# Performance work log

Measured on AMD Instinct MI355X. Metric: run time of the kernel, lower is better.

The kernel has to match this reference:

```python
import jax, jax.numpy as jnp
import numpy as np
import math

B, Q_LEN, PAST, HID = 1, 1024, 3072, 4096
NH, NKV, HD = 32, 8, 128
KV_LEN = PAST + Q_LEN
ROPE_THETA = 10000.0


def setup_inputs() -> dict:
    key = jax.random.key(0)
    ks = jax.random.split(key, 8)
    s = 0.02
    hidden_states = jax.random.normal(ks[0], (B, Q_LEN, HID), jnp.float32)
    # additive causal mask with KV cache offset: query i attends keys j <= PAST + i
    i = jnp.arange(Q_LEN)[:, None]
    j = jnp.arange(KV_LEN)[None, :]
    attention_mask = jnp.where(j <= PAST + i, 0.0, -1e9).astype(jnp.float32)[None, None]
    position_ids = (jnp.arange(Q_LEN, dtype=jnp.int64) + PAST)[None, :]
    past_k = jax.random.normal(ks[1], (B, NKV, PAST, HD), jnp.float32)
    past_v = jax.random.normal(ks[2], (B, NKV, PAST, HD), jnp.float32)
    Wq = jax.random.normal(ks[3], (NH * HD, HID), jnp.float32) * s
    Wk = jax.random.normal(ks[4], (NKV * HD, HID), jnp.float32) * s
    Wv = jax.random.normal(ks[5], (NKV * HD, HID), jnp.float32) * s
    Wo = jax.random.normal(ks[6], (HID, NH * HD), jnp.float32) * s
    return {"hidden_states": hidden_states, "attention_mask": attention_mask,
            "position_ids": position_ids, "past_k": past_k, "past_v": past_v,
            "Wq": Wq, "Wk": Wk, "Wv": Wv, "Wo": Wo}


def _rope_tables(seq_len, head_dim, dtype):
    inv_freq = 1.0 / (ROPE_THETA ** (jnp.arange(0, head_dim, 2, dtype=jnp.float32) / head_dim))
    t = jnp.arange(seq_len, dtype=jnp.float32)
    freqs = jnp.outer(t, inv_freq)            # [seq, hd/2]
    emb = jnp.concatenate([freqs, freqs], -1)  # [seq, hd]
    return jnp.cos(emb).astype(dtype), jnp.sin(emb).astype(dtype)


def _rotate_half(x):
    x1, x2 = jnp.split(x, 2, axis=-1)
    return jnp.concatenate([-x2, x1], axis=-1)


def reference(hidden_states, attention_mask, position_ids, past_k, past_v, Wq, Wk, Wv, Wo):
    bsz, q_len, _ = hidden_states.shape
    q = (hidden_states @ Wq.T).reshape(bsz, q_len, NH, HD).transpose(0, 2, 1, 3)
    k = (hidden_states @ Wk.T).reshape(bsz, q_len, NKV, HD).transpose(0, 2, 1, 3)
    v = (hidden_states @ Wv.T).reshape(bsz, q_len, NKV, HD).transpose(0, 2, 1, 3)

    kv_seq_len = q_len + past_k.shape[2]
    cos_t, sin_t = _rope_tables(kv_seq_len, HD, q.dtype)
    cos = cos_t[position_ids][:, None]  # [b,1,q,hd]
    sin = sin_t[position_ids][:, None]
    q = q * cos + _rotate_half(q) * sin
    k = k * cos + _rotate_half(k) * sin

    k = jnp.concatenate([past_k, k], axis=2)  # [b,nkv,kv,hd]
    v = jnp.concatenate([past_v, v], axis=2)
    n_rep = NH // NKV
    k = jnp.repeat(k, n_rep, axis=1)  # GQA repeat_kv -> [b,nh,kv,hd]
    v = jnp.repeat(v, n_rep, axis=1)

    scores = jnp.einsum('bhqd,bhkd->bhqk', q, k) / math.sqrt(HD)
    scores = scores + attention_mask
    weights = jax.nn.softmax(scores.astype(jnp.float32), axis=-1).astype(q.dtype)
    attn = jnp.einsum('bhqk,bhkd->bhqd', weights, v)
    attn = attn.transpose(0, 2, 1, 3).reshape(bsz, q_len, NH * HD)
    return attn @ Wo.T
```

## Files before the change

### kernel.cpp

```cpp
#include <hip/hip_runtime.h>

#define QLEN 1024
#define PASTN 3072
#define KVLEN 4096
#define HIDN 4096
#define NHEAD 32
#define NKVH 8
#define HDIM 128
#define NQKVC 6144

typedef unsigned short u16;
typedef __bf16 bf16x8 __attribute__((ext_vector_type(8)));
typedef float f32x4 __attribute__((ext_vector_type(4)));
typedef float f32x16 __attribute__((ext_vector_type(16)));
typedef u16 us8 __attribute__((ext_vector_type(8)));
typedef u16 us4 __attribute__((ext_vector_type(4)));

__device__ __forceinline__ u16 f2bf(float x) {
  unsigned u = __builtin_bit_cast(unsigned, x);
  u += 0x7fffu + ((u >> 16) & 1u);
  return (u16)(u >> 16);
}
__device__ __forceinline__ float bf2f(u16 b) {
  return __builtin_bit_cast(float, (unsigned)b << 16);
}

#define GLL16(gp, lp) __builtin_amdgcn_global_load_lds( \
    (const __attribute__((address_space(1))) void*)(gp), \
    (__attribute__((address_space(3))) void*)(lp), 16, 0, 0)

__global__ __launch_bounds__(256) void cvt_kernel(const float* __restrict__ src,
                                                  u16* __restrict__ dst, int n) {
  int i = (blockIdx.x * 256 + threadIdx.x) * 4;
  if (i >= n) return;
  float4 f = *(const float4*)(src + i);
  ushort4 o = make_ushort4(f2bf(f.x), f2bf(f.y), f2bf(f.z), f2bf(f.w));
  *(ushort4*)(dst + i) = o;
}

__device__ __forceinline__ void storeC(float* p, float v) { *p = v; }
__device__ __forceinline__ void storeC(u16* p, float v) { *p = f2bf(v); }

template <typename CT>
__global__ __launch_bounds__(256) void gemm_bt(const u16* __restrict__ A,
                                               const u16* __restrict__ B,
                                               CT* __restrict__ C, int M, int N, int K) {
  __shared__ u16 Alds[2][64 * 32];
  __shared__ u16 Blds[2][128 * 32];
  const int tid = threadIdx.x, wid = tid >> 6, lane = tid & 63;
  const int m0 = blockIdx.y * 64, n0 = blockIdx.x * 128;
  const int wm = (wid >> 1) * 32, wn = (wid & 1) * 64;
  const int l15 = lane & 15, l4 = lane >> 4;
  const int srow = lane >> 2, sp = lane & 3;
  f32x4 acc[2][4] = {};
  auto stage = [&](int buf, int kt) {
    {
      const int r = wid * 16 + srow;
      GLL16(A + (size_t)(m0 + r) * K + kt + (sp ^ ((r >> 1) & 3)) * 8,
            &Alds[buf][wid * 512]);
    }
#pragma unroll
    for (int i = 0; i < 2; ++i) {
      const int c = wid * 2 + i;
      const int r = c * 16 + srow;
      GLL16(B + (size_t)(n0 + r) * K + kt + (sp ^ ((r >> 1) & 3)) * 8,
            &Blds[buf][c * 512]);
    }
  };
  stage(0, 0);
  __syncthreads();
  int cur = 0;
  for (int kt = 0; kt < K; kt += 32) {
    if (kt + 32 < K) stage(cur ^ 1, kt + 32);
    bf16x8 a[2], b[4];
#pragma unroll
    for (int i = 0; i < 2; ++i) {
      const int R = wm + i * 16 + l15;
      a[i] = *(const bf16x8*)&Alds[cur][R * 32 + (l4 ^ ((R >> 1) & 3)) * 8];
    }
#pragma unroll
    for (int j = 0; j < 4; ++j) {
      const int R = wn + j * 16 + l15;
      b[j] = *(const bf16x8*)&Blds[cur][R * 32 + (l4 ^ ((R >> 1) & 3)) * 8];
    }
#pragma unroll
    for (int i = 0; i < 2; ++i)
#pragma unroll
      for (int j = 0; j < 4; ++j)
        acc[i][j] = __builtin_amdgcn_mfma_f32_16x16x32_bf16(a[i], b[j], acc[i][j], 0, 0, 0);
    __syncthreads();
    cur ^= 1;
  }
#pragma unroll
  for (int i = 0; i < 2; ++i)
#pragma unroll
    for (int j = 0; j < 4; ++j) {
      int row = m0 + wm + i * 16 + l4 * 4;
      int col = n0 + wn + j * 16 + l15;
#pragma unroll
      for (int r = 0; r < 4; ++r) storeC(&C[(size_t)(row + r) * N + col], acc[i][j][r]);
    }
}

__global__ __launch_bounds__(256) void rope_q_kernel(const u16* __restrict__ qkv,
                                                     u16* __restrict__ qr) {
  int idx = blockIdx.x * 256 + threadIdx.x;
  int i = idx & 63, h = (idx >> 6) & 31, r = idx >> 11;
  float freq = __expf(-(float)i * (9.210340371976184f / 64.f));
  float angle = (float)(PASTN + r) * freq;
  float sn, cs;
  sincosf(angle, &sn, &cs);
  int base = r * NQKVC + h * HDIM + i;
  float x1 = bf2f(qkv[base]);
  float x2 = bf2f(qkv[base + 64]);
  int ob = r * HIDN + h * HDIM + i;
  qr[ob] = f2bf(x1 * cs - x2 * sn);
  qr[ob + 64] = f2bf(x2 * cs + x1 * sn);
}

__global__ __launch_bounds__(256) void repack_k_kernel(const float* __restrict__ past_k,
                                                       const u16* __restrict__ qkv,
                                                       u16* __restrict__ kb) {
  int idx = blockIdx.x * 256 + threadIdx.x;
  int d = idx & 127, kv = (idx >> 7) & 4095, hk = idx >> 19;
  float val;
  if (kv < PASTN) {
    val = past_k[((size_t)hk * PASTN + kv) * HDIM + d];
  } else {
    int r = kv - PASTN;
    float x = bf2f(qkv[(size_t)r * NQKVC + 4096 + hk * HDIM + d]);
    float xp = bf2f(qkv[(size_t)r * NQKVC + 4096 + hk * HDIM + (d ^ 64)]);
    int i = d & 63;
    float freq = __expf(-(float)i * (9.210340371976184f / 64.f));
    float angle = (float)(PASTN + r) * freq;
    float sn, cs;
    sincosf(angle, &sn, &cs);
    val = (d < 64) ? (x * cs - xp * sn) : (x * cs + xp * sn);
  }
  kb[idx] = f2bf(val);
}

__global__ __launch_bounds__(256) void repack_vt_kernel(const float* __restrict__ past_v,
                                                        const u16* __restrict__ qkv,
                                                        u16* __restrict__ vtb) {
  __shared__ u16 tile[32][136];
  int hk = blockIdx.y, kv0 = blockIdx.x * 32, tid = threadIdx.x;
  int j = tid >> 3, d0 = (tid & 7) * 16;
  if (kv0 < PASTN) {
    const float* src = past_v + ((size_t)hk * PASTN + kv0 + j) * HDIM + d0;
#pragma unroll
    for (int x = 0; x < 16; x += 4) {
      float4 f = *(const float4*)(src + x);
      tile[j][d0 + x] = f2bf(f.x);
      tile[j][d0 + x + 1] = f2bf(f.y);
      tile[j][d0 + x + 2] = f2bf(f.z);
      tile[j][d0 + x + 3] = f2bf(f.w);
    }
  } else {
    int r = kv0 - PASTN + j;
    const u16* src = qkv + (size_t)r * NQKVC + 5120 + hk * HDIM + d0;
    *(us8*)&tile[j][d0] = *(const us8*)src;
    *(us8*)&tile[j][d0 + 8] = *(const us8*)(src + 8);
  }
  __syncthreads();
  int d = tid >> 1, jb = (tid & 1) * 16;
  us8 o0, o1;
#pragma unroll
  for (int x = 0; x < 8; ++x) {
    o0[x] = tile[jb + x][d];
    o1[x] = tile[jb + 8 + x][d];
  }
  u16* dst = vtb + ((size_t)hk * HDIM + d) * KVLEN + kv0 + jb;
  *(us8*)dst = o0;
  *(us8*)(dst + 8) = o1;
}

__global__ __launch_bounds__(128) void attn_kernel(const u16* __restrict__ q,
                                                   const u16* __restrict__ kc,
                                                   const u16* __restrict__ vt,
                                                   float* __restrict__ opart,
                                                   float* __restrict__ mlbuf) {
  __shared__ u16 Klds[64 * 128];
  __shared__ u16 Vlds[128 * 64];
  const int tid = threadIdx.x, wid = tid >> 6, lane = tid & 63;
  const int l31 = lane & 31, hi = lane >> 5, l15 = lane & 15;
  const int h = blockIdx.y, hk = h >> 2;
  const int q0 = blockIdx.x * 64;
  const int z = blockIdx.z;
  const int pid = h * 16 + blockIdx.x;
  const int qrow = q0 + wid * 32 + l31;
  bf16x8 qf[8];
  {
    const u16* qp = q + (size_t)qrow * HIDN + h * HDIM + hi * 8;
#pragma unroll
    for (int dk = 0; dk < 8; ++dk) qf[dk] = *(const bf16x8*)(qp + dk * 16);
  }
  float m_run = -1e30f, l_run = 0.f;
  f32x16 oacc[4] = {};
  const u16* kbase = kc + (size_t)hk * KVLEN * HDIM;
  const u16* vbase = vt + (size_t)hk * HDIM * KVLEN;
  const int ntiles = (PASTN + q0 + 64) >> 6;
  const int half = ntiles >> 1;
  const int t0 = z ? half : 0, t1 = z ? ntiles : half;
  const float C = 0.12753102f;
  const int qpos = PASTN + qrow;
  for (int t = t0; t < t1; ++t) {
    const int kv0 = t << 6;
    {
#pragma unroll
      for (int i = 0; i < 8; ++i) {
        const int w = wid * 8 + i;
        const int p = w * 4 + (lane >> 4);
        const int key = (p & 0x33) | ((p & 4) << 1) | ((p & 8) >> 1);
        const int sl = (lane & 15) ^ (p & 15);
        GLL16(kbase + (size_t)(kv0 + key) * HDIM + sl * 8, &Klds[w * 512]);
      }
#pragma unroll
      for (int i = 0; i < 8; ++i) {
        const int w = wid * 8 + i;
        const int d = w * 8 + (lane >> 3);
        const int sl = (lane & 7) ^ ((lane >> 3) & 7);
        GLL16(vbase + (size_t)d * KVLEN + kv0 + sl * 8, &Vlds[w * 512]);
      }
    }
    __syncthreads();
    f32x16 s[2] = {};
    __builtin_amdgcn_s_setprio(1);
#pragma unroll
    for (int tt = 0; tt < 2; ++tt)
#pragma unroll
      for (int dk = 0; dk < 8; ++dk) {
        const int idx = (tt * 32 + l31) * 128 + (((dk * 2 + hi) ^ l15) * 8);
        bf16x8 kf = *(const bf16x8*)&Klds[idx];
        s[tt] = __builtin_amdgcn_mfma_f32_32x32x16_bf16(kf, qf[dk], s[tt], 0, 0, 0);
      }
    __builtin_amdgcn_s_setprio(0);
    float pm = -1e30f;
    if (t == ntiles - 1) {
#pragma unroll
      for (int tt = 0; tt < 2; ++tt)
#pragma unroll
        for (int reg = 0; reg < 16; ++reg) {
          const int key = kv0 + tt * 32 + (reg & 7) + 8 * hi + ((reg & 8) << 1);
          float v = s[tt][reg] * C;
          if (key > qpos) v = -1e30f;
          s[tt][reg] = v;
          pm = fmaxf(pm, v);
        }
    } else {
#pragma unroll
      for (int tt = 0; tt < 2; ++tt)
#pragma unroll
        for (int reg = 0; reg < 16; ++reg) {
          float v = s[tt][reg] * C;
          s[tt][reg] = v;
          pm = fmaxf(pm, v);
        }
    }
    pm = fmaxf(pm, __shfl_xor(pm, 32));
    if (!__all(pm <= m_run)) {
      const float mn = fmaxf(m_run, pm);
      const float corr = exp2f(m_run - mn);
      m_run = mn;
      l_run *= corr;
#pragma unroll
      for (int db = 0; db < 4; ++db)
#pragma unroll
        for (int r = 0; r < 16; ++r) oacc[db][r] *= corr;
    }
    float rs = 0.f;
#pragma unroll
    for (int tt = 0; tt < 2; ++tt)
#pragma unroll
      for (int reg = 0; reg < 16; ++reg) {
        const float p = exp2f(s[tt][reg] - m_run);
        s[tt][reg] = p;
        rs += p;
      }
    rs += __shfl_xor(rs, 32);
    l_run += rs;
    __builtin_amdgcn_s_setprio(1);
#pragma unroll
    for (int kc2 = 0; kc2 < 4; ++kc2) {
      bf16x8 pa;
#pragma unroll
      for (int j = 0; j < 8; ++j) pa[j] = (__bf16)s[kc2 >> 1][(kc2 & 1) * 8 + j];
#pragma unroll
      for (int db = 0; db < 4; ++db) {
        const int idx = (db * 32 + l31) * 64 + (((kc2 * 2 + hi) ^ (l31 & 7)) * 8);
        bf16x8 vf = *(const bf16x8*)&Vlds[idx];
        oacc[db] = __builtin_amdgcn_mfma_f32_32x32x16_bf16(vf, pa, oacc[db], 0, 0, 0);
      }
    }
    __builtin_amdgcn_s_setprio(0);
    __syncthreads();
  }
  const int orow = wid * 32 + l31;
  float* op = opart + (size_t)(z * 512 + pid) * (64 * 128) + orow * 128;
#pragma unroll
  for (int db = 0; db < 4; ++db)
#pragma unroll
    for (int g = 0; g < 4; ++g) {
      f32x4 w4;
#pragma unroll
      for (int j = 0; j < 4; ++j) w4[j] = oacc[db][g * 4 + j];
      *(f32x4*)&op[db * 32 + g * 8 + hi * 4] = w4;
    }
  if (hi == 0) {
    float* mlp = mlbuf + (size_t)((z * 512 + pid) * 64 + orow) * 2;
    mlp[0] = m_run;
    mlp[1] = l_run;
  }
}

__global__ __launch_bounds__(256) void attn_combine(const float* __restrict__ opart,
                                                    const float* __restrict__ mlbuf,
                                                    u16* __restrict__ o) {
  const int pid = blockIdx.x;
  const int h = pid >> 4, qt = pid & 15;
  const int q = threadIdx.x >> 2, dc = (threadIdx.x & 3) * 32;
  const float* ml0 = mlbuf + (size_t)(pid * 64 + q) * 2;
  const float* ml1 = mlbuf + (size_t)((512 + pid) * 64 + q) * 2;
  const float m0 = ml0[0], l0 = ml0[1], m1 = ml1[0], l1 = ml1[1];
  const float m = fmaxf(m0, m1);
  const float w0 = exp2f(m0 - m), w1 = exp2f(m1 - m);
  const float inv = 1.f / (w0 * l0 + w1 * l1);
  const float* O0 = opart + (size_t)pid * (64 * 128) + q * 128 + dc;
  const float* O1 = opart + (size_t)(512 + pid) * (64 * 128) + q * 128 + dc;
  u16* dst = o + (size_t)(qt * 64 + q) * HIDN + h * HDIM + dc;
#pragma unroll
  for (int x = 0; x < 8; ++x) {
    f32x4 a = *(const f32x4*)(O0 + x * 4);
    f32x4 b = *(const f32x4*)(O1 + x * 4);
    us4 w4;
#pragma unroll
    for (int j = 0; j < 4; ++j) w4[j] = f2bf((a[j] * w0 + b[j] * w1) * inv);
    *(us4*)(dst + x * 4) = w4;
  }
}

extern "C" void kernel_launch(void* const* d_in, const int* in_sizes, int n_in,
                              void* d_out, int out_size, void* d_ws, size_t ws_size,
                              hipStream_t stream) {
  (void)in_sizes; (void)n_in; (void)out_size; (void)ws_size;
  const float* hidden = (const float*)d_in[0];
  const float* past_k = (const float*)d_in[3];
  const float* past_v = (const float*)d_in[4];
  const float* Wq = (const float*)d_in[5];
  const float* Wk = (const float*)d_in[6];
  const float* Wv = (const float*)d_in[7];
  const float* Wo = (const float*)d_in[8];
  float* out = (float*)d_out;

  char* w = (char*)d_ws;
  u16* hiddenb = (u16*)w; w += (size_t)QLEN * HIDN * 2;
  u16* wqkv    = (u16*)w; w += (size_t)NQKVC * HIDN * 2;
  u16* wo      = (u16*)w; w += (size_t)HIDN * HIDN * 2;
  u16* qkvraw  = (u16*)w; w += (size_t)QLEN * NQKVC * 2;
  u16* qrope   = (u16*)w; w += (size_t)QLEN * HIDN * 2;
  u16* kbuf    = (u16*)w; w += (size_t)NKVH * KVLEN * HDIM * 2;
  u16* vtbuf   = (u16*)w; w += (size_t)NKVH * HDIM * KVLEN * 2;
  u16* attnb   = (u16*)w; w += (size_t)QLEN * HIDN * 2;
  float* opart = (float*)wqkv;
  float* mlbuf = opart + (size_t)2 * 512 * 64 * 128;

  cvt_kernel<<<(QLEN * HIDN) / 1024, 256, 0, stream>>>(hidden, hiddenb, QLEN * HIDN);
  cvt_kernel<<<(NHEAD * HDIM * HIDN) / 1024, 256, 0, stream>>>(Wq, wqkv, NHEAD * HDIM * HIDN);
  cvt_kernel<<<(NKVH * HDIM * HIDN) / 1024, 256, 0, stream>>>(Wk, wqkv + (size_t)4096 * HIDN,
                                                              NKVH * HDIM * HIDN);
  cvt_kernel<<<(NKVH * HDIM * HIDN) / 1024, 256, 0, stream>>>(Wv, wqkv + (size_t)5120 * HIDN,
                                                              NKVH * HDIM * HIDN);
  cvt_kernel<<<(HIDN * HIDN) / 1024, 256, 0, stream>>>(Wo, wo, HIDN * HIDN);

  gemm_bt<u16><<<dim3(NQKVC / 128, QLEN / 64), 256, 0, stream>>>(hiddenb, wqkv, qkvraw,
                                                                 QLEN, NQKVC, HIDN);

  rope_q_kernel<<<(QLEN * NHEAD * 64) / 256, 256, 0, stream>>>(qkvraw, qrope);
  repack_k_kernel<<<(NKVH * KVLEN * HDIM) / 256, 256, 0, stream>>>(past_k, qkvraw, kbuf);
  repack_vt_kernel<<<dim3(KVLEN / 32, NKVH), 256, 0, stream>>>(past_v, qkvraw, vtbuf);

  attn_kernel<<<dim3(QLEN / 64, NHEAD, 2), 128, 0, stream>>>(qrope, kbuf, vtbuf,
                                                             opart, mlbuf);
  attn_combine<<<512, 256, 0, stream>>>(opart, mlbuf, attnb);

  gemm_bt<float><<<dim3(HIDN / 128, QLEN / 64), 256, 0, stream>>>(attnb, wo, out,
                                                                  QLEN, HIDN, HIDN);
}
```

Measured before the change: 381.9 us.

## Enlarge attention query tile to 256 rows and double-buffer K/V staging

Each attention block now handles 256 query rows with 8 waves instead of 64 rows with 2 waves, so every K/V tile staged in LDS is reused by four times as many queries. Global-to-LDS loads for the next tile are prefetched into a second LDS buffer while the current one is computed, overlapping load latency with MFMA work. The causal mask test now covers the last several tiles, because rows earlier in a larger block reach the diagonal sooner, and the combine kernel and partial-buffer layout are reshaped to match. In exchange, the grid shrinks to 256 blocks, roughly one per CU, which lowers latency hiding across blocks, and LDS use per block doubles.

```diff
diff --git a/kernel.cpp b/kernel.cpp
--- a/kernel.cpp
+++ b/kernel.cpp
@@ -175,19 +175,19 @@
   *(us8*)(dst + 8) = o1;
 }
 
-__global__ __launch_bounds__(128) void attn_kernel(const u16* __restrict__ q,
+__global__ __launch_bounds__(512) void attn_kernel(const u16* __restrict__ q,
                                                    const u16* __restrict__ kc,
                                                    const u16* __restrict__ vt,
                                                    float* __restrict__ opart,
                                                    float* __restrict__ mlbuf) {
-  __shared__ u16 Klds[64 * 128];
-  __shared__ u16 Vlds[128 * 64];
+  __shared__ u16 Klds[2][64 * 128];
+  __shared__ u16 Vlds[2][128 * 64];
   const int tid = threadIdx.x, wid = tid >> 6, lane = tid & 63;
   const int l31 = lane & 31, hi = lane >> 5, l15 = lane & 15;
   const int h = blockIdx.y, hk = h >> 2;
-  const int q0 = blockIdx.x * 64;
+  const int q0 = blockIdx.x * 256;
   const int z = blockIdx.z;
-  const int pid = h * 16 + blockIdx.x;
+  const int pid = h * 4 + blockIdx.x;
   const int qrow = q0 + wid * 32 + l31;
   bf16x8 qf[8];
   {
@@ -199,31 +199,36 @@
   f32x16 oacc[4] = {};
   const u16* kbase = kc + (size_t)hk * KVLEN * HDIM;
   const u16* vbase = vt + (size_t)hk * HDIM * KVLEN;
-  const int ntiles = (PASTN + q0 + 64) >> 6;
+  const int ntiles = (PASTN + q0 + 256) >> 6;
   const int half = ntiles >> 1;
   const int t0 = z ? half : 0, t1 = z ? ntiles : half;
   const float C = 0.12753102f;
   const int qpos = PASTN + qrow;
+  auto stage = [&](int buf, int kv0) {
+#pragma unroll
+    for (int i = 0; i < 2; ++i) {
+      const int w = wid * 2 + i;
+      const int p = w * 4 + (lane >> 4);
+      const int key = (p & 0x33) | ((p & 4) << 1) | ((p & 8) >> 1);
+      const int sl = (lane & 15) ^ (p & 15);
+      GLL16(kbase + (size_t)(kv0 + key) * HDIM + sl * 8, &Klds[buf][w * 512]);
+    }
+#pragma unroll
+    for (int i = 0; i < 2; ++i) {
+      const int w = wid * 2 + i;
+      const int d = w * 8 + (lane >> 3);
+      const int sl = (lane & 7) ^ ((lane >> 3) & 7);
+      GLL16(vbase + (size_t)d * KVLEN + kv0 + sl * 8, &Vlds[buf][w * 512]);
+    }
+  };
+  stage(0, t0 << 6);
+  __syncthreads();
+  int cur = 0;
   for (int t = t0; t < t1; ++t) {
+    if (t + 1 < t1) stage(cur ^ 1, (t + 1) << 6);
     const int kv0 = t << 6;
-    {
-#pragma unroll
-      for (int i = 0; i < 8; ++i) {
-        const int w = wid * 8 + i;
-        const int p = w * 4 + (lane >> 4);
-        const int key = (p & 0x33) | ((p & 4) << 1) | ((p & 8) >> 1);
-        const int sl = (lane & 15) ^ (p & 15);
-        GLL16(kbase + (size_t)(kv0 + key) * HDIM + sl * 8, &Klds[w * 512]);
-      }
-#pragma unroll
-      for (int i = 0; i < 8; ++i) {
-        const int w = wid * 8 + i;
-        const int d = w * 8 + (lane >> 3);
-        const int sl = (lane & 7) ^ ((lane >> 3) & 7);
-        GLL16(vbase + (size_t)d * KVLEN + kv0 + sl * 8, &Vlds[w * 512]);
-      }
-    }
-    __syncthreads();
+    const u16* Kb = Klds[cur];
+    const u16* Vb = Vlds[cur];
     f32x16 s[2] = {};
     __builtin_amdgcn_s_setprio(1);
 #pragma unroll
@@ -231,12 +236,12 @@
 #pragma unroll
       for (int dk = 0; dk < 8; ++dk) {
         const int idx = (tt * 32 + l31) * 128 + (((dk * 2 + hi) ^ l15) * 8);
-        bf16x8 kf = *(const bf16x8*)&Klds[idx];
+        bf16x8 kf = *(const bf16x8*)&Kb[idx];
         s[tt] = __builtin_amdgcn_mfma_f32_32x32x16_bf16(kf, qf[dk], s[tt], 0, 0, 0);
       }
     __builtin_amdgcn_s_setprio(0);
     float pm = -1e30f;
-    if (t == ntiles - 1) {
+    if (kv0 + 63 > PASTN + q0) {
 #pragma unroll
       for (int tt = 0; tt < 2; ++tt)
 #pragma unroll
@@ -288,15 +293,16 @@
 #pragma unroll
       for (int db = 0; db < 4; ++db) {
         const int idx = (db * 32 + l31) * 64 + (((kc2 * 2 + hi) ^ (l31 & 7)) * 8);
-        bf16x8 vf = *(const bf16x8*)&Vlds[idx];
+        bf16x8 vf = *(const bf16x8*)&Vb[idx];
         oacc[db] = __builtin_amdgcn_mfma_f32_32x32x16_bf16(vf, pa, oacc[db], 0, 0, 0);
       }
     }
     __builtin_amdgcn_s_setprio(0);
     __syncthreads();
+    cur ^= 1;
   }
   const int orow = wid * 32 + l31;
-  float* op = opart + (size_t)(z * 512 + pid) * (64 * 128) + orow * 128;
+  float* op = opart + ((size_t)(z * 128 + pid) * 256 + orow) * 128;
 #pragma unroll
   for (int db = 0; db < 4; ++db)
 #pragma unroll
@@ -307,7 +313,7 @@
       *(f32x4*)&op[db * 32 + g * 8 + hi * 4] = w4;
     }
   if (hi == 0) {
-    float* mlp = mlbuf + (size_t)((z * 512 + pid) * 64 + orow) * 2;
+    float* mlp = mlbuf + ((size_t)(z * 128 + pid) * 256 + orow) * 2;
     mlp[0] = m_run;
     mlp[1] = l_run;
   }
@@ -317,25 +323,29 @@
                                                     const float* __restrict__ mlbuf,
                                                     u16* __restrict__ o) {
   const int pid = blockIdx.x;
-  const int h = pid >> 4, qt = pid & 15;
-  const int q = threadIdx.x >> 2, dc = (threadIdx.x & 3) * 32;
-  const float* ml0 = mlbuf + (size_t)(pid * 64 + q) * 2;
-  const float* ml1 = mlbuf + (size_t)((512 + pid) * 64 + q) * 2;
-  const float m0 = ml0[0], l0 = ml0[1], m1 = ml1[0], l1 = ml1[1];
-  const float m = fmaxf(m0, m1);
-  const float w0 = exp2f(m0 - m), w1 = exp2f(m1 - m);
-  const float inv = 1.f / (w0 * l0 + w1 * l1);
-  const float* O0 = opart + (size_t)pid * (64 * 128) + q * 128 + dc;
-  const float* O1 = opart + (size_t)(512 + pid) * (64 * 128) + q * 128 + dc;
-  u16* dst = o + (size_t)(qt * 64 + q) * HIDN + h * HDIM + dc;
-#pragma unroll
-  for (int x = 0; x < 8; ++x) {
-    f32x4 a = *(const f32x4*)(O0 + x * 4);
-    f32x4 b = *(const f32x4*)(O1 + x * 4);
-    us4 w4;
-#pragma unroll
-    for (int j = 0; j < 4; ++j) w4[j] = f2bf((a[j] * w0 + b[j] * w1) * inv);
-    *(us4*)(dst + x * 4) = w4;
+  const int h = pid >> 2, qt = pid & 3;
+  const int q2 = threadIdx.x >> 2, dc = (threadIdx.x & 3) * 32;
+#pragma unroll
+  for (int b = 0; b < 4; ++b) {
+    const int q = b * 64 + q2;
+    const float* ml0 = mlbuf + ((size_t)pid * 256 + q) * 2;
+    const float* ml1 = mlbuf + ((size_t)(128 + pid) * 256 + q) * 2;
+    const float m0 = ml0[0], l0 = ml0[1], m1 = ml1[0], l1 = ml1[1];
+    const float m = fmaxf(m0, m1);
+    const float w0 = exp2f(m0 - m), w1 = exp2f(m1 - m);
+    const float inv = 1.f / (w0 * l0 + w1 * l1);
+    const float* O0 = opart + ((size_t)pid * 256 + q) * 128 + dc;
+    const float* O1 = opart + ((size_t)(128 + pid) * 256 + q) * 128 + dc;
+    u16* dst = o + (size_t)(qt * 256 + q) * HIDN + h * HDIM + dc;
+#pragma unroll
+    for (int x = 0; x < 8; ++x) {
+      f32x4 a = *(const f32x4*)(O0 + x * 4);
+      f32x4 bb = *(const f32x4*)(O1 + x * 4);
+      us4 w4;
+#pragma unroll
+      for (int j = 0; j < 4; ++j) w4[j] = f2bf((a[j] * w0 + bb[j] * w1) * inv);
+      *(us4*)(dst + x * 4) = w4;
+    }
   }
 }
 
@@ -362,7 +372,7 @@
   u16* vtbuf   = (u16*)w; w += (size_t)NKVH * HDIM * KVLEN * 2;
   u16* attnb   = (u16*)w; w += (size_t)QLEN * HIDN * 2;
   float* opart = (float*)wqkv;
-  float* mlbuf = opart + (size_t)2 * 512 * 64 * 128;
+  float* mlbuf = opart + (size_t)2 * 128 * 256 * 128;
 
   cvt_kernel<<<(QLEN * HIDN) / 1024, 256, 0, stream>>>(hidden, hiddenb, QLEN * HIDN);
   cvt_kernel<<<(NHEAD * HDIM * HIDN) / 1024, 256, 0, stream>>>(Wq, wqkv, NHEAD * HDIM * HIDN);
@@ -379,9 +389,9 @@
   repack_k_kernel<<<(NKVH * KVLEN * HDIM) / 256, 256, 0, stream>>>(past_k, qkvraw, kbuf);
   repack_vt_kernel<<<dim3(KVLEN / 32, NKVH), 256, 0, stream>>>(past_v, qkvraw, vtbuf);
 
-  attn_kernel<<<dim3(QLEN / 64, NHEAD, 2), 128, 0, stream>>>(qrope, kbuf, vtbuf,
-                                                             opart, mlbuf);
-  attn_combine<<<512, 256, 0, stream>>>(opart, mlbuf, attnb);
+  attn_kernel<<<dim3(QLEN / 256, NHEAD, 2), 512, 0, stream>>>(qrope, kbuf, vtbuf,
+                                                              opart, mlbuf);
+  attn_combine<<<128, 256, 0, stream>>>(opart, mlbuf, attnb);
 
   gemm_bt<float><<<dim3(HIDN / 128, QLEN / 64), 256, 0, stream>>>(attnb, wo, out,
                                                                   QLEN, HIDN, HIDN);
```

After: 344.6 us. 9.8% less time.
